# Optimization experiments

Hardware: AMD Instinct MI355X
Metric: run time of the kernel (lower is better)

The kernel has to match this reference:

```python
import jax, jax.numpy as jnp
import numpy as np

N, M, D = 16384, 4096, 128
NEG = -1e30  # masked-score fill


def setup_inputs() -> dict:
    key = jax.random.key(0)
    k1, k2, k3, k4 = jax.random.split(key, 4)
    self_feats = jax.random.normal(k1, (N, D), dtype=jnp.float32)
    features_neighs = jax.random.normal(k2, (M, D), dtype=jnp.float32)
    neigh_matrix = jax.random.randint(k3, (N, M), 0, 2, dtype=jnp.int32)
    # xavier_uniform for a: shape (2D, 1), gain=1 -> limit = sqrt(6/(2D+1))
    limit = float(np.sqrt(6.0 / (2 * D + 1)))
    a = jax.random.uniform(k4, (2 * D, 1), minval=-limit, maxval=limit, dtype=jnp.float32)
    return {"self_feats": self_feats, "features_neighs": features_neighs,
            "neigh_matrix": neigh_matrix, "a": a}


def reference(self_feats, features_neighs, neigh_matrix, a):
    # a = [a_self; a_neigh]; cat([self_i, neigh_j]) @ a = self_i@a_self + neigh_j@a_neigh
    d = self_feats.shape[1]
    s_self = self_feats @ a[:d, 0]        # [N]
    s_neigh = features_neighs @ a[d:, 0]  # [M]
    scores = jax.nn.leaky_relu(s_self[:, None] + s_neigh[None, :], 0.2)  # [N, M]
    mask = neigh_matrix.astype(bool)
    scores = jnp.where(mask, scores, NEG)
    attn = jax.nn.softmax(scores, axis=1)          # masked softmax per node
    attn = jnp.where(mask, attn, 0.0)              # nodes with no neighbors -> zeros
    return attn @ features_neighs                  # [N, D] weighted neighbor sum
```

## Files before the change

### kernel.cpp

```cpp
#include <hip/hip_runtime.h>
#include <hip/hip_bf16.h>

#define NROWS 16384
#define MCOLS 4096
#define DDIM  128
#define LOG2E 1.4426950408889634f

typedef __attribute__((ext_vector_type(8))) short short8;
typedef __attribute__((ext_vector_type(4))) float f32x4;

__device__ __forceinline__ float wave_reduce_add(float d) {
#pragma unroll
  for (int off = 32; off >= 1; off >>= 1) d += __shfl_xor(d, off, 64);
  return d;
}

__device__ __forceinline__ float pcalc(float t, int m) {
  float u = fmaxf(t, 0.2f * t);
  float e = exp2f(u);
  return m != 0 ? e : 0.f;
}

__device__ __forceinline__ unsigned short f2bf(float f) {
  unsigned u = __builtin_bit_cast(unsigned, f);
  return (unsigned short)((u + 0x7fffu + ((u >> 16) & 1u)) >> 16);
}

__device__ __forceinline__ unsigned pack_bf2(float lo, float hi) {
  return (unsigned)f2bf(lo) | ((unsigned)f2bf(hi) << 16);
}

__global__ __launch_bounds__(256) void aggr_prep(
    const float* __restrict__ V, const float* __restrict__ a,
    float* __restrict__ sneigh, short* __restrict__ packedV) {
  const int t = threadIdx.x, lane = t & 63, w = t >> 6;
  const int blk = blockIdx.x;

  float a0 = a[DDIM + 2 * lane] * LOG2E;
  float a1 = a[DDIM + 2 * lane + 1] * LOG2E;
#pragma unroll
  for (int i = 0; i < 4; ++i) {
    int j = blk * 16 + w * 4 + i;
    float2 v = *(const float2*)(V + (long)j * DDIM + 2 * lane);
    float d = wave_reduce_add(v.x * a0 + v.y * a1);
    if (lane == 0) sneigh[j] = d;
  }

  const int tg = blk * 256 + t;
  const int l = tg & 63;
  const int chunkid = tg >> 6;
  const int c = chunkid & 15, kt = chunkid >> 4;
  const int ks2 = c >> 3, cf = c & 7;
  const int col = cf * 16 + (l & 15);
  const long krow = (long)kt * 64 + ks2 * 32 + (l >> 4) * 8;
  short8 o;
#pragma unroll
  for (int b = 0; b < 8; ++b) {
    float f = V[(krow + b) * DDIM + col];
    o[b] = (short)f2bf(f);
  }
  *(short8*)(packedV + (long)tg * 8) = o;
}

__global__ __launch_bounds__(256, 3) void aggr_main(
    const float* __restrict__ self_feats, const int* __restrict__ nm,
    const float* __restrict__ a, const float* __restrict__ sneigh,
    const short* __restrict__ packedV, float* __restrict__ out) {
  __shared__ float s_sn[MCOLS];
  __shared__ float s_ss[64];
  __shared__ __align__(16) short Bst[2][8192];

  const int t = threadIdx.x, lane = t & 63, w = t >> 6;
  const int blk = blockIdx.x;
  const int rowblk = blk * 64;
  const int arow = lane & 15, kg = lane >> 4;

  {
    float a0 = a[2 * lane] * LOG2E, a1 = a[2 * lane + 1] * LOG2E;
#pragma unroll
    for (int i = 0; i < 16; ++i) {
      int r = w * 16 + i;
      float2 v = *(const float2*)(self_feats + (long)(rowblk + r) * DDIM + 2 * lane);
      float d = wave_reduce_add(v.x * a0 + v.y * a1);
      if (lane == 0) s_ss[r] = d;
    }
  }
  {
    const float4* src = (const float4*)sneigh;
    float4* dst = (float4*)s_sn;
    dst[t] = src[t];
    dst[t + 256] = src[t + 256];
    dst[t + 512] = src[t + 512];
    dst[t + 768] = src[t + 768];
  }

  auto STAGE = [&](int buf, int kt) {
#pragma unroll
    for (int j = 0; j < 4; ++j) {
      int c = w * 4 + j;
      const short* g = packedV + ((long)(kt * 16 + c) * 64 + lane) * 8;
      __builtin_amdgcn_global_load_lds(
          (const __attribute__((address_space(1))) void*)g,
          (__attribute__((address_space(3))) void*)(&Bst[buf][c * 512]),
          16, 0, 0);
    }
  };

  const int* mbase = nm + (long)(rowblk + w * 16 + arow) * MCOLS + kg * 8;

  int4 mc[4], mn[4] = {};
  STAGE(0, 0);
#pragma unroll
  for (int ks2 = 0; ks2 < 2; ++ks2)
#pragma unroll
    for (int q = 0; q < 2; ++q)
      mc[ks2 * 2 + q] = *(const int4*)(mbase + ks2 * 32 + q * 4);
  __syncthreads();

  const float si = s_ss[w * 16 + arow];

  f32x4 acc[8];
#pragma unroll
  for (int i = 0; i < 8; ++i) acc[i] = (f32x4){0.f, 0.f, 0.f, 0.f};
  float den = 0.f;

#pragma unroll 2
  for (int it = 0; it < 64; ++it) {
    const int buf = it & 1;
    if (it < 63) {
      STAGE(buf ^ 1, it + 1);
      __builtin_amdgcn_sched_barrier(0);
#pragma unroll
      for (int ks2 = 0; ks2 < 2; ++ks2)
#pragma unroll
        for (int q = 0; q < 2; ++q)
          mn[ks2 * 2 + q] = *(const int4*)(mbase + (it + 1) * 64 + ks2 * 32 + q * 4);
      __builtin_amdgcn_sched_barrier(0);
    }

    short8 afr[2];
#pragma unroll
    for (int ks2 = 0; ks2 < 2; ++ks2) {
      const float* sj = &s_sn[it * 64 + ks2 * 32 + kg * 8];
      float4 s0 = *(const float4*)sj;
      float4 s1 = *(const float4*)(sj + 4);
      int4 m0 = mc[ks2 * 2], m1 = mc[ks2 * 2 + 1];
      float p0 = pcalc(si + s0.x, m0.x);
      float p1 = pcalc(si + s0.y, m0.y);
      float p2 = pcalc(si + s0.z, m0.z);
      float p3 = pcalc(si + s0.w, m0.w);
      float p4 = pcalc(si + s1.x, m1.x);
      float p5 = pcalc(si + s1.y, m1.y);
      float p6 = pcalc(si + s1.z, m1.z);
      float p7 = pcalc(si + s1.w, m1.w);
      den += ((p0 + p1) + (p2 + p3)) + ((p4 + p5) + (p6 + p7));
      int4 ai;
      ai.x = (int)pack_bf2(p0, p1);
      ai.y = (int)pack_bf2(p2, p3);
      ai.z = (int)pack_bf2(p4, p5);
      ai.w = (int)pack_bf2(p6, p7);
      afr[ks2] = __builtin_bit_cast(short8, ai);
    }

    const short8* Bks = (const short8*)&Bst[buf][0];
#pragma unroll
    for (int cf = 0; cf < 8; ++cf) {
      acc[cf] = __builtin_amdgcn_mfma_f32_16x16x32_bf16(afr[0], Bks[cf * 64 + lane], acc[cf], 0, 0, 0);
      acc[cf] = __builtin_amdgcn_mfma_f32_16x16x32_bf16(afr[1], Bks[(8 + cf) * 64 + lane], acc[cf], 0, 0, 0);
    }

    asm volatile("s_waitcnt vmcnt(4)" ::: "memory");
    __builtin_amdgcn_sched_barrier(0);
    __builtin_amdgcn_s_barrier();
    mc[0] = mn[0]; mc[1] = mn[1]; mc[2] = mn[2]; mc[3] = mn[3];
  }

  den += __shfl_xor(den, 16, 64);
  den += __shfl_xor(den, 32, 64);

  float rcp[4];
#pragma unroll
  for (int r = 0; r < 4; ++r) {
    float dv = __shfl(den, kg * 4 + r, 64);
    rcp[r] = dv > 0.f ? 1.0f / dv : 0.f;
  }
#pragma unroll
  for (int cf = 0; cf < 8; ++cf)
#pragma unroll
    for (int r = 0; r < 4; ++r)
      out[(long)(rowblk + w * 16 + kg * 4 + r) * DDIM + cf * 16 + arow] =
          acc[cf][r] * rcp[r];
}

extern "C" void kernel_launch(void* const* d_in, const int* in_sizes, int n_in,
                              void* d_out, int out_size, void* d_ws, size_t ws_size,
                              hipStream_t stream) {
  const float* self_feats = (const float*)d_in[0];
  const float* V = (const float*)d_in[1];
  const int* nm = (const int*)d_in[2];
  const float* a = (const float*)d_in[3];
  float* out = (float*)d_out;

  float* sneigh = (float*)d_ws;
  short* packedV = (short*)((char*)d_ws + 16384);

  aggr_prep<<<256, 256, 0, stream>>>(V, a, sneigh, packedV);
  aggr_main<<<256, 256, 0, stream>>>(self_feats, nm, a, sneigh, packedV, out);
}
```

Measured before the change: 421.4 us.

## Split K across waves with 32-row blocks and deeper mask prefetch

Each block now covers 32 rows instead of 64 and the grid doubles to 512 blocks. The four waves form two row groups times two K-halves, and the K-halves are combined at the end through LDS. The mask loads are prefetched three iterations ahead through a 4-slot register ring, with the loop body unrolled by hand in a macro. The self score is computed with a per-lane dot product instead of a wave reduction. The aim is more parallelism and better hiding of the memory latency of the 256MB mask stream, at the cost of extra LDS, more registers (launch bounds lowered to 2) and a final reduction step.

```diff
diff --git a/kernel.cpp b/kernel.cpp
--- a/kernel.cpp
+++ b/kernel.cpp
@@ -62,134 +62,165 @@
   *(short8*)(packedV + (long)tg * 8) = o;
 }
 
-__global__ __launch_bounds__(256, 3) void aggr_main(
+#define BODY(I, SC, BUF, STG, MSK, VMC)                                        \
+  {                                                                            \
+    const int i_ = (I);                                                        \
+    if (STG) STAGE((BUF) ^ 1, i_ + 1);                                         \
+    __builtin_amdgcn_sched_barrier(0);                                         \
+    if (MSK) MASK((((SC) + 3) & 3), i_ + 3);                                   \
+    __builtin_amdgcn_sched_barrier(0);                                         \
+    short8 afr[2];                                                             \
+    _Pragma("unroll")                                                          \
+    for (int ks2 = 0; ks2 < 2; ++ks2) {                                        \
+      const float* sj = &s_sn[(ks * 32 + i_) * 64 + ks2 * 32 + kg * 8];        \
+      float4 s0 = *(const float4*)sj;                                          \
+      float4 s1 = *(const float4*)(sj + 4);                                    \
+      int4 m0 = rg[SC][ks2 * 2], m1 = rg[SC][ks2 * 2 + 1];                     \
+      float p0 = pcalc(si + s0.x, m0.x);                                       \
+      float p1 = pcalc(si + s0.y, m0.y);                                       \
+      float p2 = pcalc(si + s0.z, m0.z);                                       \
+      float p3 = pcalc(si + s0.w, m0.w);                                       \
+      float p4 = pcalc(si + s1.x, m1.x);                                       \
+      float p5 = pcalc(si + s1.y, m1.y);                                       \
+      float p6 = pcalc(si + s1.z, m1.z);                                       \
+      float p7 = pcalc(si + s1.w, m1.w);                                       \
+      den += ((p0 + p1) + (p2 + p3)) + ((p4 + p5) + (p6 + p7));                \
+      int4 ai;                                                                 \
+      ai.x = (int)pack_bf2(p0, p1);                                            \
+      ai.y = (int)pack_bf2(p2, p3);                                            \
+      ai.z = (int)pack_bf2(p4, p5);                                            \
+      ai.w = (int)pack_bf2(p6, p7);                                            \
+      afr[ks2] = __builtin_bit_cast(short8, ai);                               \
+    }                                                                          \
+    const short8* Bks = (const short8*)&Bst[BUF][ks][0];                       \
+    _Pragma("unroll")                                                          \
+    for (int cf = 0; cf < 8; ++cf) {                                           \
+      acc[cf] = __builtin_amdgcn_mfma_f32_16x16x32_bf16(                       \
+          afr[0], Bks[cf * 64 + lane], acc[cf], 0, 0, 0);                      \
+      acc[cf] = __builtin_amdgcn_mfma_f32_16x16x32_bf16(                       \
+          afr[1], Bks[(8 + cf) * 64 + lane], acc[cf], 0, 0, 0);                \
+    }                                                                          \
+    asm volatile("s_waitcnt vmcnt(" #VMC ")" ::: "memory");                    \
+    __builtin_amdgcn_sched_barrier(0);                                         \
+    __builtin_amdgcn_s_barrier();                                              \
+    __builtin_amdgcn_sched_barrier(0);                                         \
+  }
+
+__global__ __launch_bounds__(256, 2) void aggr_main(
     const float* __restrict__ self_feats, const int* __restrict__ nm,
     const float* __restrict__ a, const float* __restrict__ sneigh,
     const short* __restrict__ packedV, float* __restrict__ out) {
   __shared__ float s_sn[MCOLS];
-  __shared__ float s_ss[64];
-  __shared__ __align__(16) short Bst[2][8192];
+  __shared__ __align__(16) short Bst[2][2][8192];
 
   const int t = threadIdx.x, lane = t & 63, w = t >> 6;
-  const int blk = blockIdx.x;
-  const int rowblk = blk * 64;
+  const int rw = w & 1, ks = w >> 1;
+  const int rowblk = blockIdx.x * 32;
   const int arow = lane & 15, kg = lane >> 4;
-
+  const int row = rowblk + rw * 16 + arow;
+
+  float sip = 0.f;
   {
-    float a0 = a[2 * lane] * LOG2E, a1 = a[2 * lane + 1] * LOG2E;
-#pragma unroll
-    for (int i = 0; i < 16; ++i) {
-      int r = w * 16 + i;
-      float2 v = *(const float2*)(self_feats + (long)(rowblk + r) * DDIM + 2 * lane);
-      float d = wave_reduce_add(v.x * a0 + v.y * a1);
-      if (lane == 0) s_ss[r] = d;
+    const float* rp = self_feats + (long)row * DDIM + kg * 32;
+    const float* ap = a + kg * 32;
+#pragma unroll
+    for (int j = 0; j < 8; ++j) {
+      float4 v = *(const float4*)(rp + j * 4);
+      float4 av = *(const float4*)(ap + j * 4);
+      sip += v.x * av.x + v.y * av.y + v.z * av.z + v.w * av.w;
     }
   }
+  sip += __shfl_xor(sip, 16, 64);
+  sip += __shfl_xor(sip, 32, 64);
+  const float si = sip * LOG2E;
+
   {
     const float4* src = (const float4*)sneigh;
     float4* dst = (float4*)s_sn;
-    dst[t] = src[t];
-    dst[t + 256] = src[t + 256];
-    dst[t + 512] = src[t + 512];
-    dst[t + 768] = src[t + 768];
-  }
-
-  auto STAGE = [&](int buf, int kt) {
-#pragma unroll
-    for (int j = 0; j < 4; ++j) {
-      int c = w * 4 + j;
+#pragma unroll
+    for (int j = 0; j < 4; ++j) dst[t + j * 256] = src[t + j * 256];
+  }
+
+  auto STAGE = [&](int buf, int i) {
+    int kt = ks * 32 + i;
+#pragma unroll
+    for (int j = 0; j < 8; ++j) {
+      int c = rw * 8 + j;
       const short* g = packedV + ((long)(kt * 16 + c) * 64 + lane) * 8;
       __builtin_amdgcn_global_load_lds(
           (const __attribute__((address_space(1))) void*)g,
-          (__attribute__((address_space(3))) void*)(&Bst[buf][c * 512]),
+          (__attribute__((address_space(3))) void*)(&Bst[buf][ks][c * 512]),
           16, 0, 0);
     }
   };
 
-  const int* mbase = nm + (long)(rowblk + w * 16 + arow) * MCOLS + kg * 8;
-
-  int4 mc[4], mn[4] = {};
+  const int* mbase = nm + (long)row * MCOLS + ks * 2048 + kg * 8;
+  int4 rg[4][4];
+  auto MASK = [&](int slot, int i) {
+#pragma unroll
+    for (int ks2 = 0; ks2 < 2; ++ks2)
+#pragma unroll
+      for (int q = 0; q < 2; ++q)
+        rg[slot][ks2 * 2 + q] = *(const int4*)(mbase + i * 64 + ks2 * 32 + q * 4);
+  };
+
+  __builtin_amdgcn_sched_barrier(0);
   STAGE(0, 0);
-#pragma unroll
-  for (int ks2 = 0; ks2 < 2; ++ks2)
-#pragma unroll
-    for (int q = 0; q < 2; ++q)
-      mc[ks2 * 2 + q] = *(const int4*)(mbase + ks2 * 32 + q * 4);
+  MASK(0, 0);
+  MASK(1, 1);
+  MASK(2, 2);
+  __builtin_amdgcn_sched_barrier(0);
+  asm volatile("s_waitcnt vmcnt(12)" ::: "memory");
   __syncthreads();
-
-  const float si = s_ss[w * 16 + arow];
+  asm volatile("s_waitcnt vmcnt(8)" ::: "memory");
 
   f32x4 acc[8];
 #pragma unroll
   for (int i = 0; i < 8; ++i) acc[i] = (f32x4){0.f, 0.f, 0.f, 0.f};
   float den = 0.f;
 
-#pragma unroll 2
-  for (int it = 0; it < 64; ++it) {
-    const int buf = it & 1;
-    if (it < 63) {
-      STAGE(buf ^ 1, it + 1);
-      __builtin_amdgcn_sched_barrier(0);
-#pragma unroll
-      for (int ks2 = 0; ks2 < 2; ++ks2)
-#pragma unroll
-        for (int q = 0; q < 2; ++q)
-          mn[ks2 * 2 + q] = *(const int4*)(mbase + (it + 1) * 64 + ks2 * 32 + q * 4);
-      __builtin_amdgcn_sched_barrier(0);
-    }
-
-    short8 afr[2];
-#pragma unroll
-    for (int ks2 = 0; ks2 < 2; ++ks2) {
-      const float* sj = &s_sn[it * 64 + ks2 * 32 + kg * 8];
-      float4 s0 = *(const float4*)sj;
-      float4 s1 = *(const float4*)(sj + 4);
-      int4 m0 = mc[ks2 * 2], m1 = mc[ks2 * 2 + 1];
-      float p0 = pcalc(si + s0.x, m0.x);
-      float p1 = pcalc(si + s0.y, m0.y);
-      float p2 = pcalc(si + s0.z, m0.z);
-      float p3 = pcalc(si + s0.w, m0.w);
-      float p4 = pcalc(si + s1.x, m1.x);
-      float p5 = pcalc(si + s1.y, m1.y);
-      float p6 = pcalc(si + s1.z, m1.z);
-      float p7 = pcalc(si + s1.w, m1.w);
-      den += ((p0 + p1) + (p2 + p3)) + ((p4 + p5) + (p6 + p7));
-      int4 ai;
-      ai.x = (int)pack_bf2(p0, p1);
-      ai.y = (int)pack_bf2(p2, p3);
-      ai.z = (int)pack_bf2(p4, p5);
-      ai.w = (int)pack_bf2(p6, p7);
-      afr[ks2] = __builtin_bit_cast(short8, ai);
-    }
-
-    const short8* Bks = (const short8*)&Bst[buf][0];
-#pragma unroll
-    for (int cf = 0; cf < 8; ++cf) {
-      acc[cf] = __builtin_amdgcn_mfma_f32_16x16x32_bf16(afr[0], Bks[cf * 64 + lane], acc[cf], 0, 0, 0);
-      acc[cf] = __builtin_amdgcn_mfma_f32_16x16x32_bf16(afr[1], Bks[(8 + cf) * 64 + lane], acc[cf], 0, 0, 0);
-    }
-
-    asm volatile("s_waitcnt vmcnt(4)" ::: "memory");
-    __builtin_amdgcn_sched_barrier(0);
-    __builtin_amdgcn_s_barrier();
-    mc[0] = mn[0]; mc[1] = mn[1]; mc[2] = mn[2]; mc[3] = mn[3];
-  }
+  for (int it = 0; it < 28; it += 4) {
+    BODY(it + 0, 0, 0, true, true, 4)
+    BODY(it + 1, 1, 1, true, true, 4)
+    BODY(it + 2, 2, 0, true, true, 4)
+    BODY(it + 3, 3, 1, true, true, 4)
+  }
+  BODY(28, 0, 0, true, true, 4)
+  BODY(29, 1, 1, true, false, 0)
+  BODY(30, 2, 0, true, false, 0)
+  BODY(31, 3, 1, false, false, 0)
+  __syncthreads();
 
   den += __shfl_xor(den, 16, 64);
   den += __shfl_xor(den, 32, 64);
 
-  float rcp[4];
-#pragma unroll
-  for (int r = 0; r < 4; ++r) {
-    float dv = __shfl(den, kg * 4 + r, 64);
-    rcp[r] = dv > 0.f ? 1.0f / dv : 0.f;
-  }
-#pragma unroll
-  for (int cf = 0; cf < 8; ++cf)
-#pragma unroll
-    for (int r = 0; r < 4; ++r)
-      out[(long)(rowblk + w * 16 + kg * 4 + r) * DDIM + cf * 16 + arow] =
-          acc[cf][r] * rcp[r];
+  float* comb = (float*)&Bst[0][0][0];
+  float* den_x = comb + 32 * 132;
+  if (ks == 1) {
+#pragma unroll
+    for (int cf = 0; cf < 8; ++cf)
+#pragma unroll
+      for (int r = 0; r < 4; ++r)
+        comb[(rw * 16 + kg * 4 + r) * 132 + cf * 16 + arow] = acc[cf][r];
+    if (lane < 16) den_x[rw * 16 + lane] = den;
+  }
+  __syncthreads();
+  if (ks == 0) {
+    float dtot = den + den_x[rw * 16 + arow];
+    float rcp[4];
+#pragma unroll
+    for (int r = 0; r < 4; ++r) {
+      float dv = __shfl(dtot, kg * 4 + r, 64);
+      rcp[r] = dv > 0.f ? 1.0f / dv : 0.f;
+    }
+#pragma unroll
+    for (int cf = 0; cf < 8; ++cf)
+#pragma unroll
+      for (int r = 0; r < 4; ++r)
+        out[(long)(rowblk + rw * 16 + kg * 4 + r) * DDIM + cf * 16 + arow] =
+            (acc[cf][r] + comb[(rw * 16 + kg * 4 + r) * 132 + cf * 16 + arow]) *
+            rcp[r];
+  }
 }
 
 extern "C" void kernel_launch(void* const* d_in, const int* in_sizes, int n_in,
@@ -205,5 +236,5 @@
   short* packedV = (short*)((char*)d_ws + 16384);
 
   aggr_prep<<<256, 256, 0, stream>>>(V, a, sneigh, packedV);
-  aggr_main<<<256, 256, 0, stream>>>(self_feats, nm, a, sneigh, packedV, out);
-}
+  aggr_main<<<512, 256, 0, stream>>>(self_feats, nm, a, sneigh, packedV, out);
+}
```

Result: faster. 389.7 us (-7.5%).
